# Kernel optimization log

Hardware: AMD Instinct MI355X
Metric: run time of the kernel (lower is better)

## Reference

```python
import jax, jax.numpy as jnp
import numpy as np

N_NODES = 1_000_000
BATCH = 100_000
DIM_NIG = 128
DIM_NODE = 128


def setup_inputs() -> dict:
    key = jax.random.key(0)
    ks = jax.random.split(key, 9)
    return {
        "src_node_ids": jax.random.randint(ks[0], (BATCH,), 0, N_NODES),
        "dst_node_ids": jax.random.randint(ks[1], (BATCH,), 0, N_NODES),
        "previous_embedding": jax.random.normal(ks[2], (N_NODES, DIM_NODE), jnp.float32),
        "batch_src_neighbor_embedding": jax.random.normal(ks[3], (BATCH, DIM_NIG), jnp.float32),
        "batch_dst_neighbor_embedding": jax.random.normal(ks[4], (BATCH, DIM_NIG), jnp.float32),
        # neighbor_layer: Linear(dim_nig -> dim_node); torch weight layout [out, in]
        "W_nig": jax.random.normal(ks[5], (DIM_NODE, DIM_NIG), jnp.float32) / np.sqrt(DIM_NIG),
        "b_nig": jax.random.normal(ks[6], (DIM_NODE,), jnp.float32) * 0.01,
        # node_layer: Linear(dim_node -> dim_node)
        "W_node": jax.random.normal(ks[7], (DIM_NODE, DIM_NODE), jnp.float32) / np.sqrt(DIM_NODE),
        "b_node": jax.random.normal(ks[8], (DIM_NODE,), jnp.float32) * 0.01,
    }


def _update(prev_emb, node_ids, nbr_emb, W_nig, b_nig, W_node, b_node):
    prev = jnp.take(prev_emb, node_ids, axis=0)          # [B, D] gather
    shift = nbr_emb @ W_nig.T + b_nig                    # [B, D]
    return (prev + shift) @ W_node.T + b_node + prev     # linear + residual


def reference(src_node_ids, dst_node_ids, previous_embedding,
              batch_src_neighbor_embedding, batch_dst_neighbor_embedding,
              W_nig, b_nig, W_node, b_node):
    src_emb = _update(previous_embedding, src_node_ids, batch_src_neighbor_embedding,
                      W_nig, b_nig, W_node, b_node)
    dst_emb = _update(previous_embedding, dst_node_ids, batch_dst_neighbor_embedding,
                      W_nig, b_nig, W_node, b_node)
    # clone().detach() in torch -> stop_gradient base, then scatter src then dst
    updated = jax.lax.stop_gradient(previous_embedding)
    updated = updated.at[src_node_ids].set(src_emb)
    updated = updated.at[dst_node_ids].set(dst_emb)
    return updated
```

## Files before the change

### kernel.cpp

```cpp
#include <hip/hip_runtime.h>
#include <hip/hip_bf16.h>

#define B_SZ 100000
#define NTOT 200000
#define NN   1000000
#define DIM  128

#define NB_CLAIM  782
#define NB_WFRAG  32
#define NB_PREP   (NB_CLAIM + NB_WFRAG + 1)

#define TILES     62500
#define GRID_MAIN 512
#define BLK_MAIN  512
#define WAVES_TOT (GRID_MAIN * 8)

typedef short bf16x8 __attribute__((ext_vector_type(8)));
typedef float f32x4  __attribute__((ext_vector_type(4)));

__device__ __forceinline__ short f2bf(float f) {
    union { float f; unsigned u; } v; v.f = f;
    unsigned u = v.u;
    u += 0x7fffu + ((u >> 16) & 1u);
    return (short)(u >> 16);
}

__device__ __forceinline__ bf16x8 cvt8(float4 a, float4 b) {
    bf16x8 r;
    r[0]=f2bf(a.x); r[1]=f2bf(a.y); r[2]=f2bf(a.z); r[3]=f2bf(a.w);
    r[4]=f2bf(b.x); r[5]=f2bf(b.y); r[6]=f2bf(b.z); r[7]=f2bf(b.w);
    return r;
}

__global__ __launch_bounds__(256) void k_prep(
        const int* __restrict__ src, const int* __restrict__ dst,
        int* __restrict__ owner,
        const float* __restrict__ Wnig, const float* __restrict__ bnig,
        const float* __restrict__ Wnode, const float* __restrict__ bnode,
        short* __restrict__ PA, short* __restrict__ PQ,
        float* __restrict__ cvec) {
    int b = blockIdx.x, t = threadIdx.x;
    if (b < NB_CLAIM) {
        int i = b * 256 + t;
        if (i < NTOT) {
            int node = (i < B_SZ) ? src[i] : dst[i - B_SZ];
            atomicMax(&owner[node], i);
        }
    } else if (b < NB_CLAIM + NB_WFRAG) {
        int b2 = b - NB_CLAIM;
        int lane = t & 63, ig = t >> 6;
        int kc = b2 >> 3, nc = b2 & 7;
        int n = nc * 16 + (lane & 15);
        int kbase = kc * 32 + (lane >> 4) * 8;
        int fo = (b2 * 64 + lane) * 8;
        for (int ii = 0; ii < 2; ++ii) {
            int i = ig * 2 + ii;
            int k = kbase + i;
            float a = Wnode[n * DIM + k] + (k == n ? 1.0f : 0.0f);
            PA[fo + i] = f2bf(a);
            float q = 0.f;
            for (int m = 0; m < DIM; ++m) q += Wnode[n * DIM + m] * Wnig[m * DIM + k];
            PQ[fo + i] = f2bf(q);
        }
    } else {
        if (t < DIM) {
            float c = bnode[t];
            for (int k = 0; k < DIM; ++k) c += bnig[k] * Wnode[t * DIM + k];
            cvec[t] = c;
        }
    }
}

__global__ __launch_bounds__(BLK_MAIN, 4) void k_node(
        const float* __restrict__ prev,
        const float* __restrict__ nsrc, const float* __restrict__ ndst,
        const int* __restrict__ owner,
        const short* __restrict__ PA, const short* __restrict__ PQ,
        const float* __restrict__ cvec,
        float* __restrict__ out) {
    __shared__ __align__(16) short lA[32 * 64 * 8];
    __shared__ __align__(16) short lQ[32 * 64 * 8];
    int tid = threadIdx.x;
    {
        const float4* gA = (const float4*)PA;
        const float4* gQ = (const float4*)PQ;
        float4* sA = (float4*)lA;
        float4* sQ = (float4*)lQ;
        for (int i = tid; i < 2048; i += BLK_MAIN) { sA[i] = gA[i]; sQ[i] = gQ[i]; }
    }
    __syncthreads();

    int wave = tid >> 6, lane = tid & 63;
    int wid = blockIdx.x * 8 + wave;
    int myrow = lane & 15;
    int koff  = (lane >> 4) * 8;
    int col0  = lane & 15;
    int rbase = (lane >> 4) * 4;

    float cv[8];
#pragma unroll
    for (int nc = 0; nc < 8; ++nc) cv[nc] = cvec[nc * 16 + col0];

    int t = wid;
    if (t >= TILES) return;
    int o_cur = owner[t * 16 + myrow];

    for (; t < TILES; t += WAVES_TOT) {
        int tn = t + WAVES_TOT;
        int o_nxt = (tn < TILES) ? owner[tn * 16 + myrow] : -1;

        int nbase = t * 16;
        const float* prow = prev + (size_t)(nbase + myrow) * DIM + koff;
        float4 pc[8];
#pragma unroll
        for (int kc = 0; kc < 4; ++kc) {
            pc[2*kc]   = *(const float4*)(prow + kc * 32);
            pc[2*kc+1] = *(const float4*)(prow + kc * 32 + 4);
        }
        bool touched = o_cur >= 0;
        float4 nb[8];
#pragma unroll
        for (int i = 0; i < 8; ++i) nb[i] = (float4){0.f, 0.f, 0.f, 0.f};
        if (touched) {
            bool is_src = o_cur < B_SZ;
            int bi = is_src ? o_cur : o_cur - B_SZ;
            const float* nrow = (is_src ? nsrc : ndst) + (size_t)bi * DIM + koff;
#pragma unroll
            for (int kc = 0; kc < 4; ++kc) {
                nb[2*kc]   = *(const float4*)(nrow + kc * 32);
                nb[2*kc+1] = *(const float4*)(nrow + kc * 32 + 4);
            }
        }
        unsigned mask16 = (unsigned)__ballot(touched) & 0xFFFFu;

        if (!touched) {
            float* orow = out + (size_t)(nbase + myrow) * DIM + koff;
#pragma unroll
            for (int kc = 0; kc < 4; ++kc) {
                *(float4*)(orow + kc * 32)     = pc[2*kc];
                *(float4*)(orow + kc * 32 + 4) = pc[2*kc+1];
            }
        }

        if (mask16) {
            f32x4 acc[8];
#pragma unroll
            for (int nc = 0; nc < 8; ++nc) acc[nc] = (f32x4){0.f, 0.f, 0.f, 0.f};
#pragma unroll
            for (int kc = 0; kc < 4; ++kc) {
                bf16x8 aP = cvt8(pc[2*kc], pc[2*kc+1]);
                bf16x8 aN = cvt8(nb[2*kc], nb[2*kc+1]);
#pragma unroll
                for (int nc = 0; nc < 8; ++nc) {
                    int fo = ((kc * 8 + nc) * 64 + lane) * 8;
                    bf16x8 bA = *(const bf16x8*)(lA + fo);
                    bf16x8 bQ = *(const bf16x8*)(lQ + fo);
                    acc[nc] = __builtin_amdgcn_mfma_f32_16x16x32_bf16(aP, bA, acc[nc], 0, 0, 0);
                    acc[nc] = __builtin_amdgcn_mfma_f32_16x16x32_bf16(aN, bQ, acc[nc], 0, 0, 0);
                }
            }
#pragma unroll
            for (int r = 0; r < 4; ++r) {
                int rt = rbase + r;
                if ((mask16 >> rt) & 1u) {
                    float* orow = out + (size_t)(nbase + rt) * DIM;
#pragma unroll
                    for (int nc = 0; nc < 8; ++nc)
                        orow[nc * 16 + col0] = acc[nc][r] + cv[nc];
                }
            }
        }
        o_cur = o_nxt;
    }
}

extern "C" void kernel_launch(void* const* d_in, const int* in_sizes, int n_in,
                              void* d_out, int out_size, void* d_ws, size_t ws_size,
                              hipStream_t stream) {
    const int*   src  = (const int*)d_in[0];
    const int*   dst  = (const int*)d_in[1];
    const float* prev = (const float*)d_in[2];
    const float* nsrc = (const float*)d_in[3];
    const float* ndst = (const float*)d_in[4];
    const float* Wnig = (const float*)d_in[5];
    const float* bnig = (const float*)d_in[6];
    const float* Wnode = (const float*)d_in[7];
    const float* bnode = (const float*)d_in[8];
    float* out = (float*)d_out;

    const size_t OWNER_B = (size_t)NN * 4;
    const size_t PA_B = 32 * 64 * 8 * 2;
    if (ws_size < OWNER_B + 2 * PA_B + 512) return;
    char* ws = (char*)d_ws;
    int*   owner = (int*)ws;
    short* PA = (short*)(ws + OWNER_B);
    short* PQ = (short*)(ws + OWNER_B + PA_B);
    float* cvec = (float*)(ws + OWNER_B + 2 * PA_B);

    hipMemsetAsync(owner, 0xFF, OWNER_B, stream);
    k_prep<<<NB_PREP, 256, 0, stream>>>(
        src, dst, owner, Wnig, bnig, Wnode, bnode, PA, PQ, cvec);
    k_node<<<GRID_MAIN, BLK_MAIN, 0, stream>>>(
        prev, nsrc, ndst, owner, PA, PQ, cvec, out);
}
```

Measured before the change: 261.1 us.

## Software-pipeline row loads across k-chunks and use nontemporal loads/stores

Restructures the per-tile loop into four double-buffered phases. Each phase loads the next 32-column chunk of the previous-embedding and neighbor rows while converting and running MFMAs on the current chunk, and copy-through rows are written chunk by chunk. Loads of the embedding table and all output stores become nontemporal to avoid polluting caches with streamed data. This cuts live registers and overlaps memory latency with compute. In exchange, fewer loads are in flight per wave at once, which could hurt a bandwidth-bound stream.

```diff
diff --git a/kernel.cpp b/kernel.cpp
--- a/kernel.cpp
+++ b/kernel.cpp
@@ -25,10 +25,10 @@
     return (short)(u >> 16);
 }
 
-__device__ __forceinline__ bf16x8 cvt8(float4 a, float4 b) {
+__device__ __forceinline__ bf16x8 cvt8(f32x4 a, f32x4 b) {
     bf16x8 r;
-    r[0]=f2bf(a.x); r[1]=f2bf(a.y); r[2]=f2bf(a.z); r[3]=f2bf(a.w);
-    r[4]=f2bf(b.x); r[5]=f2bf(b.y); r[6]=f2bf(b.z); r[7]=f2bf(b.w);
+    r[0]=f2bf(a[0]); r[1]=f2bf(a[1]); r[2]=f2bf(a[2]); r[3]=f2bf(a[3]);
+    r[4]=f2bf(b[0]); r[5]=f2bf(b[1]); r[6]=f2bf(b[2]); r[7]=f2bf(b[3]);
     return r;
 }
 
@@ -105,68 +105,81 @@
     if (t >= TILES) return;
     int o_cur = owner[t * 16 + myrow];
 
+    const f32x4 z = (f32x4){0.f, 0.f, 0.f, 0.f};
+
     for (; t < TILES; t += WAVES_TOT) {
         int tn = t + WAVES_TOT;
         int o_nxt = (tn < TILES) ? owner[tn * 16 + myrow] : -1;
 
         int nbase = t * 16;
+        bool touched = o_cur >= 0;
         const float* prow = prev + (size_t)(nbase + myrow) * DIM + koff;
-        float4 pc[8];
-#pragma unroll
-        for (int kc = 0; kc < 4; ++kc) {
-            pc[2*kc]   = *(const float4*)(prow + kc * 32);
-            pc[2*kc+1] = *(const float4*)(prow + kc * 32 + 4);
-        }
-        bool touched = o_cur >= 0;
-        float4 nb[8];
-#pragma unroll
-        for (int i = 0; i < 8; ++i) nb[i] = (float4){0.f, 0.f, 0.f, 0.f};
+        float*       orow = out  + (size_t)(nbase + myrow) * DIM + koff;
+        const float* nrow = nullptr;
         if (touched) {
             bool is_src = o_cur < B_SZ;
             int bi = is_src ? o_cur : o_cur - B_SZ;
-            const float* nrow = (is_src ? nsrc : ndst) + (size_t)bi * DIM + koff;
-#pragma unroll
-            for (int kc = 0; kc < 4; ++kc) {
-                nb[2*kc]   = *(const float4*)(nrow + kc * 32);
-                nb[2*kc+1] = *(const float4*)(nrow + kc * 32 + 4);
-            }
+            nrow = (is_src ? nsrc : ndst) + (size_t)bi * DIM + koff;
         }
         unsigned mask16 = (unsigned)__ballot(touched) & 0xFFFFu;
 
-        if (!touched) {
-            float* orow = out + (size_t)(nbase + myrow) * DIM + koff;
-#pragma unroll
-            for (int kc = 0; kc < 4; ++kc) {
-                *(float4*)(orow + kc * 32)     = pc[2*kc];
-                *(float4*)(orow + kc * 32 + 4) = pc[2*kc+1];
-            }
-        }
+        f32x4 pA0, pA1, nA0, nA1, pB0, pB1, nB0, nB1;
+        pA0 = __builtin_nontemporal_load((const f32x4*)prow);
+        pA1 = __builtin_nontemporal_load((const f32x4*)(prow + 4));
+        nA0 = z; nA1 = z;
+        if (touched) {
+            nA0 = *(const f32x4*)nrow;
+            nA1 = *(const f32x4*)(nrow + 4);
+        }
+
+        f32x4 acc[8];
+#pragma unroll
+        for (int nc = 0; nc < 8; ++nc) acc[nc] = z;
+
+#define PHASE(KC, PC0, PC1, NC0, NC1, PN0, PN1, NN0, NN1)                          \
+        {                                                                          \
+            if ((KC) < 3) {                                                        \
+                PN0 = __builtin_nontemporal_load((const f32x4*)(prow + ((KC)+1)*32));     \
+                PN1 = __builtin_nontemporal_load((const f32x4*)(prow + ((KC)+1)*32 + 4)); \
+                NN0 = z; NN1 = z;                                                  \
+                if (touched) {                                                     \
+                    NN0 = *(const f32x4*)(nrow + ((KC)+1)*32);                     \
+                    NN1 = *(const f32x4*)(nrow + ((KC)+1)*32 + 4);                 \
+                }                                                                  \
+            }                                                                      \
+            if (!touched) {                                                        \
+                __builtin_nontemporal_store(PC0, (f32x4*)(orow + (KC)*32));        \
+                __builtin_nontemporal_store(PC1, (f32x4*)(orow + (KC)*32 + 4));    \
+            }                                                                      \
+            if (mask16) {                                                          \
+                bf16x8 aP = cvt8(PC0, PC1);                                        \
+                bf16x8 aN = cvt8(NC0, NC1);                                        \
+                _Pragma("unroll")                                                  \
+                for (int nc = 0; nc < 8; ++nc) {                                   \
+                    int fo = (((KC) * 8 + nc) * 64 + lane) * 8;                    \
+                    bf16x8 bA = *(const bf16x8*)(lA + fo);                         \
+                    bf16x8 bQ = *(const bf16x8*)(lQ + fo);                         \
+                    acc[nc] = __builtin_amdgcn_mfma_f32_16x16x32_bf16(aP, bA, acc[nc], 0, 0, 0); \
+                    acc[nc] = __builtin_amdgcn_mfma_f32_16x16x32_bf16(aN, bQ, acc[nc], 0, 0, 0); \
+                }                                                                  \
+            }                                                                      \
+        }
+
+        PHASE(0, pA0, pA1, nA0, nA1, pB0, pB1, nB0, nB1)
+        PHASE(1, pB0, pB1, nB0, nB1, pA0, pA1, nA0, nA1)
+        PHASE(2, pA0, pA1, nA0, nA1, pB0, pB1, nB0, nB1)
+        PHASE(3, pB0, pB1, nB0, nB1, pA0, pA1, nA0, nA1)
+#undef PHASE
 
         if (mask16) {
-            f32x4 acc[8];
-#pragma unroll
-            for (int nc = 0; nc < 8; ++nc) acc[nc] = (f32x4){0.f, 0.f, 0.f, 0.f};
-#pragma unroll
-            for (int kc = 0; kc < 4; ++kc) {
-                bf16x8 aP = cvt8(pc[2*kc], pc[2*kc+1]);
-                bf16x8 aN = cvt8(nb[2*kc], nb[2*kc+1]);
-#pragma unroll
-                for (int nc = 0; nc < 8; ++nc) {
-                    int fo = ((kc * 8 + nc) * 64 + lane) * 8;
-                    bf16x8 bA = *(const bf16x8*)(lA + fo);
-                    bf16x8 bQ = *(const bf16x8*)(lQ + fo);
-                    acc[nc] = __builtin_amdgcn_mfma_f32_16x16x32_bf16(aP, bA, acc[nc], 0, 0, 0);
-                    acc[nc] = __builtin_amdgcn_mfma_f32_16x16x32_bf16(aN, bQ, acc[nc], 0, 0, 0);
-                }
-            }
 #pragma unroll
             for (int r = 0; r < 4; ++r) {
                 int rt = rbase + r;
                 if ((mask16 >> rt) & 1u) {
-                    float* orow = out + (size_t)(nbase + rt) * DIM;
+                    float* ow = out + (size_t)(nbase + rt) * DIM;
 #pragma unroll
                     for (int nc = 0; nc < 8; ++nc)
-                        orow[nc * 16 + col0] = acc[nc][r] + cv[nc];
+                        __builtin_nontemporal_store(acc[nc][r] + cv[nc], &ow[nc * 16 + col0]);
                 }
             }
         }
```

Result: slower. 266.8 us (+2.2%).

## Compact touched rows per 32-row supertile before MFMA and coalesce copy-through

Applied to the files above, without the earlier changes.

Each wave now handles a 32-row supertile. It ballots which rows have an owner and compacts those rows into a per-wave shared-memory list, so the MFMA work runs only on touched rows in 16-row batches. Untouched rows are copied with fully coalesced float4 loads and stores instead of per-row strided accesses. This removes wasted MFMA work on mostly-untouched tiles and improves copy coalescing. The cost is that touched rows of prev are re-read from global memory and the list adds LDS traffic. The old prefetch of the next tile's owner is also dropped.

```diff
diff --git a/kernel.cpp b/kernel.cpp
--- a/kernel.cpp
+++ b/kernel.cpp
@@ -10,10 +10,11 @@
 #define NB_WFRAG  32
 #define NB_PREP   (NB_CLAIM + NB_WFRAG + 1)
 
-#define TILES     62500
+#define SUPER     32
+#define NSUP      31250
 #define GRID_MAIN 512
 #define BLK_MAIN  512
-#define WAVES_TOT (GRID_MAIN * 8)
+#define NWAVE     (GRID_MAIN * 8)
 
 typedef short bf16x8 __attribute__((ext_vector_type(8)));
 typedef float f32x4  __attribute__((ext_vector_type(4)));
@@ -25,10 +26,10 @@
     return (short)(u >> 16);
 }
 
-__device__ __forceinline__ bf16x8 cvt8(float4 a, float4 b) {
+__device__ __forceinline__ bf16x8 cvt8(f32x4 a, f32x4 b) {
     bf16x8 r;
-    r[0]=f2bf(a.x); r[1]=f2bf(a.y); r[2]=f2bf(a.z); r[3]=f2bf(a.w);
-    r[4]=f2bf(b.x); r[5]=f2bf(b.y); r[6]=f2bf(b.z); r[7]=f2bf(b.w);
+    r[0]=f2bf(a[0]); r[1]=f2bf(a[1]); r[2]=f2bf(a[2]); r[3]=f2bf(a[3]);
+    r[4]=f2bf(b[0]); r[5]=f2bf(b[1]); r[6]=f2bf(b[2]); r[7]=f2bf(b[3]);
     return r;
 }
 
@@ -80,6 +81,7 @@
         float* __restrict__ out) {
     __shared__ __align__(16) short lA[32 * 64 * 8];
     __shared__ __align__(16) short lQ[32 * 64 * 8];
+    __shared__ int lists[8][SUPER];
     int tid = threadIdx.x;
     {
         const float4* gA = (const float4*)PA;
@@ -91,8 +93,7 @@
     __syncthreads();
 
     int wave = tid >> 6, lane = tid & 63;
-    int wid = blockIdx.x * 8 + wave;
-    int myrow = lane & 15;
+    int* list = lists[wave];
     int koff  = (lane >> 4) * 8;
     int col0  = lane & 15;
     int rbase = (lane >> 4) * 4;
@@ -101,54 +102,74 @@
 #pragma unroll
     for (int nc = 0; nc < 8; ++nc) cv[nc] = cvec[nc * 16 + col0];
 
-    int t = wid;
-    if (t >= TILES) return;
-    int o_cur = owner[t * 16 + myrow];
-
-    for (; t < TILES; t += WAVES_TOT) {
-        int tn = t + WAVES_TOT;
-        int o_nxt = (tn < TILES) ? owner[tn * 16 + myrow] : -1;
-
-        int nbase = t * 16;
-        const float* prow = prev + (size_t)(nbase + myrow) * DIM + koff;
-        float4 pc[8];
-#pragma unroll
-        for (int kc = 0; kc < 4; ++kc) {
-            pc[2*kc]   = *(const float4*)(prow + kc * 32);
-            pc[2*kc+1] = *(const float4*)(prow + kc * 32 + 4);
-        }
-        bool touched = o_cur >= 0;
-        float4 nb[8];
-#pragma unroll
-        for (int i = 0; i < 8; ++i) nb[i] = (float4){0.f, 0.f, 0.f, 0.f};
-        if (touched) {
-            bool is_src = o_cur < B_SZ;
-            int bi = is_src ? o_cur : o_cur - B_SZ;
-            const float* nrow = (is_src ? nsrc : ndst) + (size_t)bi * DIM + koff;
+    const f32x4 z = (f32x4){0.f, 0.f, 0.f, 0.f};
+
+    for (int s = blockIdx.x * 8 + wave; s < NSUP; s += NWAVE) {
+        size_t nbase = (size_t)s * SUPER;
+
+        int own = -1;
+        if (lane < SUPER) own = owner[nbase + lane];
+        unsigned mask = (unsigned)__ballot(own >= 0);
+        int cnt = __popc(mask);
+        if (own >= 0) {
+            int rank = __popc(mask & ((1u << lane) - 1u));
+            list[rank] = (own << 5) | lane;
+        }
+
+        const f32x4* p4 = (const f32x4*)(prev + nbase * DIM);
+        f32x4*       o4 = (f32x4*)(out  + nbase * DIM);
+#pragma unroll
+        for (int half = 0; half < 2; ++half) {
+            f32x4 v[8];
+#pragma unroll
+            for (int j = 0; j < 8; ++j) v[j] = p4[(half * 8 + j) * 64 + lane];
+#pragma unroll
+            for (int j = 0; j < 8; ++j) {
+                int fi = (half * 8 + j) * 64 + lane;
+                int row = fi >> 5;
+                if (!((mask >> row) & 1u)) o4[fi] = v[j];
+            }
+        }
+
+        if (cnt == 0) continue;
+
+        const float* ps = prev + nbase * DIM;
+#pragma unroll 1
+        for (int tb = 0; tb < SUPER; tb += 16) {
+            if (cnt <= tb) break;
+            int idx = tb + (lane & 15);
+            bool act = idx < cnt;
+            int pk = act ? list[idx] : 0;
+            int arow = pk & 31;
+            int code = pk >> 5;
+
+            f32x4 nb[8];
+#pragma unroll
+            for (int i = 0; i < 8; ++i) nb[i] = z;
+            if (act) {
+                const float* nrow = (code < B_SZ
+                        ? nsrc + (size_t)code * DIM
+                        : ndst + (size_t)(code - B_SZ) * DIM) + koff;
+#pragma unroll
+                for (int kc = 0; kc < 4; ++kc) {
+                    nb[2*kc]   = *(const f32x4*)(nrow + kc * 32);
+                    nb[2*kc+1] = *(const f32x4*)(nrow + kc * 32 + 4);
+                }
+            }
+
+            f32x4 acc[8];
+#pragma unroll
+            for (int nc = 0; nc < 8; ++nc) acc[nc] = z;
+
+            const float* prow = ps + (size_t)arow * DIM + koff;
 #pragma unroll
             for (int kc = 0; kc < 4; ++kc) {
-                nb[2*kc]   = *(const float4*)(nrow + kc * 32);
-                nb[2*kc+1] = *(const float4*)(nrow + kc * 32 + 4);
-            }
-        }
-        unsigned mask16 = (unsigned)__ballot(touched) & 0xFFFFu;
-
-        if (!touched) {
-            float* orow = out + (size_t)(nbase + myrow) * DIM + koff;
-#pragma unroll
-            for (int kc = 0; kc < 4; ++kc) {
-                *(float4*)(orow + kc * 32)     = pc[2*kc];
-                *(float4*)(orow + kc * 32 + 4) = pc[2*kc+1];
-            }
-        }
-
-        if (mask16) {
-            f32x4 acc[8];
-#pragma unroll
-            for (int nc = 0; nc < 8; ++nc) acc[nc] = (f32x4){0.f, 0.f, 0.f, 0.f};
-#pragma unroll
-            for (int kc = 0; kc < 4; ++kc) {
-                bf16x8 aP = cvt8(pc[2*kc], pc[2*kc+1]);
+                f32x4 a0 = z, a1 = z;
+                if (act) {
+                    a0 = *(const f32x4*)(prow + kc * 32);
+                    a1 = *(const f32x4*)(prow + kc * 32 + 4);
+                }
+                bf16x8 aP = cvt8(a0, a1);
                 bf16x8 aN = cvt8(nb[2*kc], nb[2*kc+1]);
 #pragma unroll
                 for (int nc = 0; nc < 8; ++nc) {
@@ -159,18 +180,19 @@
                     acc[nc] = __builtin_amdgcn_mfma_f32_16x16x32_bf16(aN, bQ, acc[nc], 0, 0, 0);
                 }
             }
+
 #pragma unroll
             for (int r = 0; r < 4; ++r) {
-                int rt = rbase + r;
-                if ((mask16 >> rt) & 1u) {
-                    float* orow = out + (size_t)(nbase + rt) * DIM;
+                int i2 = tb + rbase + r;
+                if (i2 < cnt) {
+                    int row2 = list[i2] & 31;
+                    float* ow = out + (nbase + row2) * DIM;
 #pragma unroll
                     for (int nc = 0; nc < 8; ++nc)
-                        orow[nc * 16 + col0] = acc[nc][r] + cv[nc];
-                }
-            }
-        }
-        o_cur = o_nxt;
+                        ow[nc * 16 + col0] = acc[nc][r] + cv[nc];
+                }
+            }
+        }
     }
 }
 
```

New measurement: 1.027 ms. 3.93x slower.

## Coalesce prev tile loads/stores and stage bf16 A-fragments through LDS

Applied to the files above, without the earlier changes.

Each wave now reads and writes its 16-row tile of prev as fully contiguous float4s across lanes, instead of per-row strided fragment loads and stores. When any row in the tile is touched, it packs the values to bf16 into a padded per-wave LDS staging buffer and reads the MFMA A-fragments back from there. The block grows to 1024 threads (16 waves) with half as many blocks. The goal is better coalescing on the dominant copy traffic, at the cost of extra LDS use and possibly lower occupancy.

```diff
diff --git a/kernel.cpp b/kernel.cpp
--- a/kernel.cpp
+++ b/kernel.cpp
@@ -11,9 +11,11 @@
 #define NB_PREP   (NB_CLAIM + NB_WFRAG + 1)
 
 #define TILES     62500
-#define GRID_MAIN 512
-#define BLK_MAIN  512
-#define WAVES_TOT (GRID_MAIN * 8)
+#define GRID_MAIN 256
+#define BLK_MAIN  1024
+#define WPB       16
+#define WAVES_TOT (GRID_MAIN * WPB)
+#define SSTRIDE   272
 
 typedef short bf16x8 __attribute__((ext_vector_type(8)));
 typedef float f32x4  __attribute__((ext_vector_type(4)));
@@ -25,11 +27,8 @@
     return (short)(u >> 16);
 }
 
-__device__ __forceinline__ bf16x8 cvt8(float4 a, float4 b) {
-    bf16x8 r;
-    r[0]=f2bf(a.x); r[1]=f2bf(a.y); r[2]=f2bf(a.z); r[3]=f2bf(a.w);
-    r[4]=f2bf(b.x); r[5]=f2bf(b.y); r[6]=f2bf(b.z); r[7]=f2bf(b.w);
-    return r;
+__device__ __forceinline__ unsigned pk2(float a, float b) {
+    return (unsigned)(unsigned short)f2bf(a) | ((unsigned)(unsigned short)f2bf(b) << 16);
 }
 
 __global__ __launch_bounds__(256) void k_prep(
@@ -80,6 +79,7 @@
         float* __restrict__ out) {
     __shared__ __align__(16) short lA[32 * 64 * 8];
     __shared__ __align__(16) short lQ[32 * 64 * 8];
+    __shared__ __align__(16) char  stg[WPB * 16 * SSTRIDE];
     int tid = threadIdx.x;
     {
         const float4* gA = (const float4*)PA;
@@ -91,11 +91,14 @@
     __syncthreads();
 
     int wave = tid >> 6, lane = tid & 63;
-    int wid = blockIdx.x * 8 + wave;
-    int myrow = lane & 15;
+    int wid = blockIdx.x * WPB + wave;
+    int p     = lane >> 5;
+    int c     = lane & 31;
     int koff  = (lane >> 4) * 8;
     int col0  = lane & 15;
     int rbase = (lane >> 4) * 4;
+    char* wstg = stg + wave * (16 * SSTRIDE);
+    const char* ard = wstg + (lane & 15) * SSTRIDE + (lane >> 4) * 16;
 
     float cv[8];
 #pragma unroll
@@ -103,53 +106,65 @@
 
     int t = wid;
     if (t >= TILES) return;
-    int o_cur = owner[t * 16 + myrow];
+    int o_cur = owner[t * 16 + (lane & 15)];
+
+    const f32x4 z = (f32x4){0.f, 0.f, 0.f, 0.f};
 
     for (; t < TILES; t += WAVES_TOT) {
         int tn = t + WAVES_TOT;
-        int o_nxt = (tn < TILES) ? owner[tn * 16 + myrow] : -1;
+        int o_nxt = (tn < TILES) ? owner[tn * 16 + (lane & 15)] : -1;
 
         int nbase = t * 16;
-        const float* prow = prev + (size_t)(nbase + myrow) * DIM + koff;
-        float4 pc[8];
-#pragma unroll
-        for (int kc = 0; kc < 4; ++kc) {
-            pc[2*kc]   = *(const float4*)(prow + kc * 32);
-            pc[2*kc+1] = *(const float4*)(prow + kc * 32 + 4);
-        }
         bool touched = o_cur >= 0;
-        float4 nb[8];
-#pragma unroll
-        for (int i = 0; i < 8; ++i) nb[i] = (float4){0.f, 0.f, 0.f, 0.f};
+        unsigned mask16 = (unsigned)(__ballot(touched) & 0xFFFFu);
+
+        f32x4 nb[8];
+#pragma unroll
+        for (int i = 0; i < 8; ++i) nb[i] = z;
         if (touched) {
             bool is_src = o_cur < B_SZ;
             int bi = is_src ? o_cur : o_cur - B_SZ;
             const float* nrow = (is_src ? nsrc : ndst) + (size_t)bi * DIM + koff;
 #pragma unroll
             for (int kc = 0; kc < 4; ++kc) {
-                nb[2*kc]   = *(const float4*)(nrow + kc * 32);
-                nb[2*kc+1] = *(const float4*)(nrow + kc * 32 + 4);
-            }
-        }
-        unsigned mask16 = (unsigned)__ballot(touched) & 0xFFFFu;
-
-        if (!touched) {
-            float* orow = out + (size_t)(nbase + myrow) * DIM + koff;
-#pragma unroll
-            for (int kc = 0; kc < 4; ++kc) {
-                *(float4*)(orow + kc * 32)     = pc[2*kc];
-                *(float4*)(orow + kc * 32 + 4) = pc[2*kc+1];
-            }
+                nb[2*kc]   = *(const f32x4*)(nrow + kc * 32);
+                nb[2*kc+1] = *(const f32x4*)(nrow + kc * 32 + 4);
+            }
+        }
+
+        const f32x4* p4 = (const f32x4*)(prev + (size_t)nbase * DIM);
+        f32x4 v[8];
+#pragma unroll
+        for (int j = 0; j < 8; ++j) v[j] = p4[j * 64 + lane];
+
+        if (mask16) {
+#pragma unroll
+            for (int j = 0; j < 8; ++j) {
+                int row = 2 * j + p;
+                uint2 w = make_uint2(pk2(v[j][0], v[j][1]), pk2(v[j][2], v[j][3]));
+                *(uint2*)(wstg + row * SSTRIDE + c * 8) = w;
+            }
+        }
+
+        f32x4* o4 = (f32x4*)(out + (size_t)nbase * DIM);
+#pragma unroll
+        for (int j = 0; j < 8; ++j) {
+            int row = 2 * j + p;
+            if (!((mask16 >> row) & 1u)) o4[j * 64 + lane] = v[j];
         }
 
         if (mask16) {
             f32x4 acc[8];
 #pragma unroll
-            for (int nc = 0; nc < 8; ++nc) acc[nc] = (f32x4){0.f, 0.f, 0.f, 0.f};
+            for (int nc = 0; nc < 8; ++nc) acc[nc] = z;
 #pragma unroll
             for (int kc = 0; kc < 4; ++kc) {
-                bf16x8 aP = cvt8(pc[2*kc], pc[2*kc+1]);
-                bf16x8 aN = cvt8(nb[2*kc], nb[2*kc+1]);
+                bf16x8 aP = *(const bf16x8*)(ard + kc * 64);
+                bf16x8 aN;
+                aN[0]=f2bf(nb[2*kc][0]); aN[1]=f2bf(nb[2*kc][1]);
+                aN[2]=f2bf(nb[2*kc][2]); aN[3]=f2bf(nb[2*kc][3]);
+                aN[4]=f2bf(nb[2*kc+1][0]); aN[5]=f2bf(nb[2*kc+1][1]);
+                aN[6]=f2bf(nb[2*kc+1][2]); aN[7]=f2bf(nb[2*kc+1][3]);
 #pragma unroll
                 for (int nc = 0; nc < 8; ++nc) {
                     int fo = ((kc * 8 + nc) * 64 + lane) * 8;
```

New measurement: 257.3 us. About the same (-1.4%).
